# Kernel optimization log

Hardware: AMD Instinct MI355X
Metric: run time of the kernel (lower is better)

## Reference

```python
import jax, jax.numpy as jnp
import numpy as np

DIM = 192
HEADS = 8
TIME = 256
HID = int(DIM * 2.66)  # 510
B, H, W = 4, 128, 128


def conv1x1(x, w, b):
    # w: [O, C], pointwise conv as einsum
    return jnp.einsum('bchw,oc->bohw', x, w) + b[None, :, None, None]


def dwconv3(x, w, b):
    # depthwise 3x3, w: [C, 1, 3, 3]
    y = jax.lax.conv_general_dilated(
        x, w, window_strides=(1, 1), padding='SAME',
        feature_group_count=x.shape[1],
        dimension_numbers=('NCHW', 'OIHW', 'NCHW'))
    return y + b[None, :, None, None]


def layernorm(x, w, b, eps=1e-6):
    # channel-wise LN; torch .std() is unbiased (ddof=1)
    C = x.shape[1]
    mean = x.mean(axis=1, keepdims=True)
    var = ((x - mean) ** 2).sum(axis=1, keepdims=True) / (C - 1)
    std = jnp.sqrt(var)
    return w * (x - mean) / (std + eps) + b


def modulate(x, t_emb, tw, tb):
    # time_mlp = Linear(SiLU(t_emb)); scale/shift conditioning
    t = jax.nn.silu(t_emb) @ tw.T + tb  # [B, 2C]
    scale, shift = jnp.split(t, 2, axis=-1)
    return x * (1.0 + scale[:, :, None, None]) + shift[:, :, None, None]


def l2norm(x, eps=1e-12):
    n = jnp.sqrt((x * x).sum(axis=-1, keepdims=True))
    return x / jnp.maximum(n, eps)


def mdta(x, t_emb, temp, qkv_w, qkv_b, dw_w, dw_b, proj_w, proj_b, tw, tb):
    Bn, C, Hh, Ww = x.shape
    x = modulate(x, t_emb, tw, tb)
    qkv = dwconv3(conv1x1(x, qkv_w, qkv_b), dw_w, dw_b)
    q, k, v = jnp.split(qkv, 3, axis=1)
    rs = lambda a: a.reshape(Bn, HEADS, C // HEADS, Hh * Ww)
    q, k, v = l2norm(rs(q)), l2norm(rs(k)), rs(v)
    attn = jnp.einsum('bhcl,bhdl->bhcd', q, k) * temp[None]  # [B,h,c,c]
    attn = jax.nn.softmax(attn, axis=-1)
    out = jnp.einsum('bhcd,bhdl->bhcl', attn, v).reshape(Bn, C, Hh, Ww)
    return conv1x1(out, proj_w, proj_b)


def gdfn(x, t_emb, c1_w, c1_b, dw_w, dw_b, c2_w, c2_b, tw, tb):
    x = modulate(x, t_emb, tw, tb)
    x = dwconv3(conv1x1(x, c1_w, c1_b), dw_w, dw_b)
    x1, x2 = jnp.split(x, 2, axis=1)
    return conv1x1(x1 * x2, c2_w, c2_b)


def setup_inputs() -> dict:
    key = jax.random.key(0)
    ks = jax.random.split(key, 16)
    s = 0.02
    d = {
        'x': jax.random.normal(ks[0], (B, DIM, H, W), jnp.float32),
        't_emb': jax.random.normal(ks[1], (B, TIME), jnp.float32),
        'n1_w': jnp.ones((1, DIM, 1, 1), jnp.float32),
        'n1_b': jnp.zeros((1, DIM, 1, 1), jnp.float32),
        'temp': jnp.ones((HEADS, 1, 1), jnp.float32),
        'a_qkv_w': jax.random.normal(ks[2], (3 * DIM, DIM), jnp.float32) * s,
        'a_qkv_b': jnp.zeros((3 * DIM,), jnp.float32),
        'a_dw_w': jax.random.normal(ks[3], (3 * DIM, 1, 3, 3), jnp.float32) * s,
        'a_dw_b': jnp.zeros((3 * DIM,), jnp.float32),
        'a_proj_w': jax.random.normal(ks[4], (DIM, DIM), jnp.float32) * s,
        'a_proj_b': jnp.zeros((DIM,), jnp.float32),
        'a_t_w': jax.random.normal(ks[5], (2 * DIM, TIME), jnp.float32) * s,
        'a_t_b': jnp.zeros((2 * DIM,), jnp.float32),
        'n2_w': jnp.ones((1, DIM, 1, 1), jnp.float32),
        'n2_b': jnp.zeros((1, DIM, 1, 1), jnp.float32),
        'f_c1_w': jax.random.normal(ks[6], (2 * HID, DIM), jnp.float32) * s,
        'f_c1_b': jnp.zeros((2 * HID,), jnp.float32),
        'f_dw_w': jax.random.normal(ks[7], (2 * HID, 1, 3, 3), jnp.float32) * s,
        'f_dw_b': jnp.zeros((2 * HID,), jnp.float32),
        'f_c2_w': jax.random.normal(ks[8], (DIM, HID), jnp.float32) * s,
        'f_c2_b': jnp.zeros((DIM,), jnp.float32),
        'f_t_w': jax.random.normal(ks[9], (2 * DIM, TIME), jnp.float32) * s,
        'f_t_b': jnp.zeros((2 * DIM,), jnp.float32),
    }
    return d


def reference(x, t_emb, n1_w, n1_b, temp, a_qkv_w, a_qkv_b, a_dw_w, a_dw_b,
              a_proj_w, a_proj_b, a_t_w, a_t_b, n2_w, n2_b,
              f_c1_w, f_c1_b, f_dw_w, f_dw_b, f_c2_w, f_c2_b, f_t_w, f_t_b):
    x = x + mdta(layernorm(x, n1_w, n1_b), t_emb, temp,
                 a_qkv_w, a_qkv_b, a_dw_w, a_dw_b, a_proj_w, a_proj_b, a_t_w, a_t_b)
    x = x + gdfn(layernorm(x, n2_w, n2_b), t_emb,
                 f_c1_w, f_c1_b, f_dw_w, f_dw_b, f_c2_w, f_c2_b, f_t_w, f_t_b)
    return x
```

## Files before the change

### kernel.cpp

```cpp
#include <hip/hip_runtime.h>
#include <math.h>

#define HW 16384

using short8 = __attribute__((ext_vector_type(8))) short;
using f32x4  = __attribute__((ext_vector_type(4))) float;

__device__ __forceinline__ float bf2f(unsigned short u){
  union { unsigned int i; float f; } x; x.i = ((unsigned int)u) << 16; return x.f;
}
__device__ __forceinline__ unsigned short f2bf(float f){
  union { float f; unsigned int i; } x; x.f = f;
  return (unsigned short)((x.i + 0x7FFFu + ((x.i >> 16) & 1u)) >> 16);
}

__global__ void castw_k(const float* __restrict__ in, unsigned short* __restrict__ out, int n){
  int i = blockIdx.x * 256 + threadIdx.x;
  if (i < n) out[i] = f2bf(in[i]);
}

__global__ void modk(const float* __restrict__ t_emb,
                     const float* __restrict__ aw, const float* __restrict__ ab,
                     const float* __restrict__ fw, const float* __restrict__ fb,
                     float* __restrict__ mod_a, float* __restrict__ mod_f){
  int o = blockIdx.x * 128 + threadIdx.x;
  int b = blockIdx.y;
  const float* w  = blockIdx.z ? fw : aw;
  const float* bi = blockIdx.z ? fb : ab;
  float* outp     = blockIdx.z ? mod_f : mod_a;
  const float* te = t_emb + b * 256;
  float acc = bi[o];
  for (int k = 0; k < 256; ++k){
    float u = te[k];
    float s = u / (1.f + expf(-u));
    acc += s * w[o * 256 + k];
  }
  outp[b * 384 + o] = acc;
}

__global__ __launch_bounds__(256) void lnmod_k(const float* __restrict__ x,
                                               const float* __restrict__ nw, const float* __restrict__ nb,
                                               const float* __restrict__ mod, unsigned short* __restrict__ y){
  int b = blockIdx.y;
  int t = threadIdx.x;
  int pl = t & 63, cg = t >> 6;
  int p = blockIdx.x * 64 + pl;
  const float* xb = x + (size_t)b * 192 * HW + p;
  float s = 0.f, s2 = 0.f;
  #pragma unroll 8
  for (int c = cg * 48; c < cg * 48 + 48; ++c){
    float v = xb[(size_t)c * HW]; s += v; s2 += v * v;
  }
  __shared__ float rs[4][64], rq[4][64];
  rs[cg][pl] = s; rq[cg][pl] = s2;
  __syncthreads();
  float S  = rs[0][pl] + rs[1][pl] + rs[2][pl] + rs[3][pl];
  float S2 = rq[0][pl] + rq[1][pl] + rq[2][pl] + rq[3][pl];
  float mean = S * (1.f / 192.f);
  float var  = (S2 - S * mean) * (1.f / 191.f);
  float rinv = 1.f / (sqrtf(fmaxf(var, 0.f)) + 1e-6f);
  const float* mo = mod + b * 384;
  unsigned short* yb = y + (size_t)b * 192 * HW + p;
  #pragma unroll 8
  for (int c = cg * 48; c < cg * 48 + 48; ++c){
    float v = xb[(size_t)c * HW];
    float ln = nw[c] * ((v - mean) * rinv) + nb[c];
    yb[(size_t)c * HW] = f2bf(ln * (1.f + mo[c]) + mo[192 + c]);
  }
}

#define BM 64
#define BN 128
#define BK 32
__global__ __launch_bounds__(256) void gemm_k(const unsigned short* __restrict__ A,
                                              const unsigned short* __restrict__ Bact,
                                              const float* __restrict__ bias,
                                              const float* resid, void* outp,
                                              int M, int K, int ofp32){
  const int N = HW;
  const unsigned short* Bp = Bact + (size_t)blockIdx.z * K * N;
  int m0 = blockIdx.y * BM, n0 = blockIdx.x * BN;
  __shared__ unsigned short As[BM][40];
  __shared__ unsigned short Bs[BK][136];
  int t = threadIdx.x;
  int wave = t >> 6, lane = t & 63;
  int wr = wave >> 1, wc = wave & 1;
  int l16 = lane & 15, quad = lane >> 4;
  f32x4 z = {0.f, 0.f, 0.f, 0.f};
  f32x4 acc[2][4];
  #pragma unroll
  for (int i = 0; i < 2; ++i)
    #pragma unroll
    for (int j = 0; j < 4; ++j) acc[i][j] = z;

  int kTiles = (K + BK - 1) / BK;
  for (int kt = 0; kt < kTiles; ++kt){
    int k0 = kt * BK;
    {
      int m = t >> 2, kk = (t & 3) * 8;
      int gm = m0 + m;
      #pragma unroll
      for (int j = 0; j < 4; ++j){
        unsigned int v = 0u;
        int gk = k0 + kk + 2 * j;
        if (gm < M && gk < K) v = *(const unsigned int*)(A + (size_t)gm * K + gk);
        *(unsigned int*)&As[m][kk + 2 * j] = v;
      }
    }
    {
      int nn = (t & 15) * 8;
      #pragma unroll
      for (int h2 = 0; h2 < 2; ++h2){
        int r = (t >> 4) + h2 * 16;
        int gk = k0 + r;
        uint4 v; v.x = v.y = v.z = v.w = 0u;
        if (gk < K) v = *(const uint4*)(Bp + (size_t)gk * N + n0 + nn);
        *(uint4*)&Bs[r][nn] = v;
      }
    }
    __syncthreads();
    short8 af[2];
    #pragma unroll
    for (int mt = 0; mt < 2; ++mt)
      af[mt] = *(const short8*)&As[wr * 32 + mt * 16 + l16][quad * 8];
    #pragma unroll
    for (int nt = 0; nt < 4; ++nt){
      int n = wc * 64 + nt * 16 + l16;
      short8 bf;
      #pragma unroll
      for (int j = 0; j < 8; ++j) bf[j] = (short)Bs[quad * 8 + j][n];
      #pragma unroll
      for (int mt = 0; mt < 2; ++mt)
        acc[mt][nt] = __builtin_amdgcn_mfma_f32_16x16x32_bf16(af[mt], bf, acc[mt][nt], 0, 0, 0);
    }
    __syncthreads();
  }
  #pragma unroll
  for (int mt = 0; mt < 2; ++mt)
    #pragma unroll
    for (int nt = 0; nt < 4; ++nt){
      int n = n0 + wc * 64 + nt * 16 + l16;
      #pragma unroll
      for (int r = 0; r < 4; ++r){
        int m = m0 + wr * 32 + mt * 16 + quad * 4 + r;
        if (m < M){
          float v = acc[mt][nt][r] + bias[m];
          size_t idx = (size_t)blockIdx.z * M * N + (size_t)m * N + n;
          if (resid) v += resid[idx];
          if (ofp32) ((float*)outp)[idx] = v;
          else       ((unsigned short*)outp)[idx] = f2bf(v);
        }
      }
    }
}

__global__ __launch_bounds__(256) void dw3_k(const unsigned short* __restrict__ in,
                                             const float* __restrict__ w, const float* __restrict__ bias,
                                             unsigned short* __restrict__ out, int C,
                                             float* __restrict__ qn, float* __restrict__ kn){
  __shared__ unsigned short tile[66 * 128];
  __shared__ float red[4];
  int zc = blockIdx.y;
  int b = zc / C, c = zc - b * C;
  int r0 = blockIdx.x * 64;
  const unsigned short* im = in + ((size_t)(b * C + c)) * HW;
  unsigned short* om = out + ((size_t)(b * C + c)) * HW;
  int t = threadIdx.x;
  #pragma unroll
  for (int i = 0; i < 5; ++i){
    int idx = t + 256 * i;
    if (idx < 1056){
      int lr = idx >> 4, lc = (idx & 15) * 8;
      int gr = r0 - 1 + lr;
      uint4 v = {0u, 0u, 0u, 0u};
      if ((unsigned)gr < 128u) v = *(const uint4*)(im + gr * 128 + lc);
      *(uint4*)&tile[lr * 128 + lc] = v;
    }
  }
  __syncthreads();
  const float* wc = w + c * 9;
  float W[9];
  #pragma unroll
  for (int i = 0; i < 9; ++i) W[i] = wc[i];
  float bs = bias[c];
  float ssq = 0.f;
  #pragma unroll
  for (int i = 0; i < 4; ++i){
    int seg = t + 256 * i;
    int orow = seg >> 4, sc = (seg & 15) * 8;
    float acc[8];
    #pragma unroll
    for (int j = 0; j < 8; ++j) acc[j] = bs;
    #pragma unroll
    for (int rr = 0; rr < 3; ++rr){
      const unsigned short* rp = &tile[(orow + rr) * 128 + sc];
      float v[10];
      v[0] = (sc > 0) ? bf2f(rp[-1]) : 0.f;
      uint4 m = *(const uint4*)rp;
      const unsigned short* mu = (const unsigned short*)&m;
      #pragma unroll
      for (int j = 0; j < 8; ++j) v[j + 1] = bf2f(mu[j]);
      v[9] = (sc < 120) ? bf2f(rp[8]) : 0.f;
      float wa = W[rr * 3], wb = W[rr * 3 + 1], wd = W[rr * 3 + 2];
      #pragma unroll
      for (int j = 0; j < 8; ++j) acc[j] += wa * v[j] + wb * v[j + 1] + wd * v[j + 2];
    }
    unsigned short ob[8];
    #pragma unroll
    for (int j = 0; j < 8; ++j){
      ob[j] = f2bf(acc[j]);
      float q = bf2f(ob[j]);
      ssq += q * q;
    }
    *(uint4*)(om + (r0 + orow) * 128 + sc) = *(uint4*)ob;
  }
  if (c < 384){
    #pragma unroll
    for (int off = 32; off; off >>= 1) ssq += __shfl_down(ssq, off);
    if ((t & 63) == 0) red[t >> 6] = ssq;
    __syncthreads();
    if (t == 0){
      float s = red[0] + red[1] + red[2] + red[3];
      float* dst = (c < 192) ? (qn + b * 192 + c) : (kn + b * 192 + c - 192);
      atomicAdd(dst, s);
    }
  }
}

__global__ __launch_bounds__(256) void dwgate_k(const unsigned short* __restrict__ h,
                                                const float* __restrict__ w, const float* __restrict__ bias,
                                                unsigned short* __restrict__ g){
  __shared__ unsigned short tile[2 * 66 * 128];
  int zc = blockIdx.y;
  int b = zc / 510, j = zc - b * 510;
  int r0 = blockIdx.x * 64;
  const unsigned short* im1 = h + ((size_t)(b * 1020 + j)) * HW;
  const unsigned short* im2 = h + ((size_t)(b * 1020 + 510 + j)) * HW;
  int t = threadIdx.x;
  #pragma unroll
  for (int i = 0; i < 9; ++i){
    int idx = t + 256 * i;
    if (idx < 2112){
      int img = (idx >= 1056) ? 1 : 0;
      int li = idx - img * 1056;
      int lr = li >> 4, lc = (li & 15) * 8;
      int gr = r0 - 1 + lr;
      uint4 v = {0u, 0u, 0u, 0u};
      const unsigned short* im = img ? im2 : im1;
      if ((unsigned)gr < 128u) v = *(const uint4*)(im + gr * 128 + lc);
      *(uint4*)&tile[img * 8448 + lr * 128 + lc] = v;
    }
  }
  __syncthreads();
  float W1[9], W2[9];
  #pragma unroll
  for (int i = 0; i < 9; ++i){ W1[i] = w[j * 9 + i]; W2[i] = w[(510 + j) * 9 + i]; }
  float b1 = bias[j], b2 = bias[510 + j];
  unsigned short* gm = g + ((size_t)(b * 510 + j)) * HW;
  #pragma unroll
  for (int i = 0; i < 4; ++i){
    int seg = t + 256 * i;
    int orow = seg >> 4, sc = (seg & 15) * 8;
    float a1[8], a2[8];
    #pragma unroll
    for (int q = 0; q < 8; ++q){ a1[q] = b1; a2[q] = b2; }
    #pragma unroll
    for (int rr = 0; rr < 3; ++rr){
      #pragma unroll
      for (int img = 0; img < 2; ++img){
        const unsigned short* rp = &tile[img * 8448 + (orow + rr) * 128 + sc];
        float v[10];
        v[0] = (sc > 0) ? bf2f(rp[-1]) : 0.f;
        uint4 m = *(const uint4*)rp;
        const unsigned short* mu = (const unsigned short*)&m;
        #pragma unroll
        for (int q = 0; q < 8; ++q) v[q + 1] = bf2f(mu[q]);
        v[9] = (sc < 120) ? bf2f(rp[8]) : 0.f;
        const float* ww = img ? W2 : W1;
        float* aa = img ? a2 : a1;
        float wa = ww[rr * 3], wb = ww[rr * 3 + 1], wd = ww[rr * 3 + 2];
        #pragma unroll
        for (int q = 0; q < 8; ++q) aa[q] += wa * v[q] + wb * v[q + 1] + wd * v[q + 2];
      }
    }
    unsigned short ob[8];
    #pragma unroll
    for (int q = 0; q < 8; ++q) ob[q] = f2bf(a1[q] * a2[q]);
    *(uint4*)(gm + (r0 + orow) * 128 + sc) = *(uint4*)ob;
  }
}

__global__ __launch_bounds__(64) void qk_k(const unsigned short* __restrict__ qkv_dw, float* __restrict__ part){
  int bh = blockIdx.y; int b = bh >> 3, h = bh & 7;
  int ks = blockIdx.x;
  int lane = threadIdx.x;
  int l16 = lane & 15, quad = lane >> 4;
  const unsigned short* qb = qkv_dw + ((size_t)b * 576 + h * 24) * HW;
  const unsigned short* kb = qkv_dw + ((size_t)b * 576 + 192 + h * 24) * HW;
  f32x4 z = {0.f, 0.f, 0.f, 0.f};
  f32x4 a00 = z, a01 = z, a10 = z, a11 = z;
  for (int st = 0; st < 16; ++st){
    int k0 = ks * 512 + st * 32 + quad * 8;
    short8 qa0 = *(const short8*)(qb + (size_t)l16 * HW + k0);
    short8 qa1 = *(const short8*)(qb + (size_t)(l16 + 16) * HW + k0);
    short8 kb0 = *(const short8*)(kb + (size_t)l16 * HW + k0);
    short8 kb1 = *(const short8*)(kb + (size_t)(l16 + 16) * HW + k0);
    a00 = __builtin_amdgcn_mfma_f32_16x16x32_bf16(qa0, kb0, a00, 0, 0, 0);
    a01 = __builtin_amdgcn_mfma_f32_16x16x32_bf16(qa0, kb1, a01, 0, 0, 0);
    a10 = __builtin_amdgcn_mfma_f32_16x16x32_bf16(qa1, kb0, a10, 0, 0, 0);
    a11 = __builtin_amdgcn_mfma_f32_16x16x32_bf16(qa1, kb1, a11, 0, 0, 0);
  }
  float* pp = part + ((size_t)bh * 32 + ks) * 576;
  #pragma unroll
  for (int r = 0; r < 4; ++r){
    int c0 = quad * 4 + r, c1 = 16 + quad * 4 + r;
    int d0 = l16, d1 = 16 + l16;
    if (c0 < 24 && d0 < 24) pp[c0 * 24 + d0] = a00[r];
    if (c0 < 24 && d1 < 24) pp[c0 * 24 + d1] = a01[r];
    if (c1 < 24 && d0 < 24) pp[c1 * 24 + d0] = a10[r];
    if (c1 < 24 && d1 < 24) pp[c1 * 24 + d1] = a11[r];
  }
}

__global__ void softmax_k(const float* __restrict__ part, const float* __restrict__ qn,
                          const float* __restrict__ kn, const float* __restrict__ temp,
                          float* __restrict__ attn){
  int bh = blockIdx.x; int b = bh >> 3, h = bh & 7;
  int c = threadIdx.x;
  if (c >= 24) return;
  float tmp = temp[h];
  float qv = fmaxf(sqrtf(qn[b * 192 + h * 24 + c]), 1e-12f);
  float row[24];
  #pragma unroll
  for (int d = 0; d < 24; ++d){
    float s = 0.f;
    for (int sp = 0; sp < 32; ++sp) s += part[((size_t)bh * 32 + sp) * 576 + c * 24 + d];
    float kv = fmaxf(sqrtf(kn[b * 192 + h * 24 + d]), 1e-12f);
    row[d] = s * tmp / (qv * kv);
  }
  float mx = row[0];
  #pragma unroll
  for (int d = 1; d < 24; ++d) mx = fmaxf(mx, row[d]);
  float sum = 0.f;
  #pragma unroll
  for (int d = 0; d < 24; ++d){ row[d] = expf(row[d] - mx); sum += row[d]; }
  float inv = 1.f / sum;
  #pragma unroll
  for (int d = 0; d < 24; ++d) attn[(size_t)bh * 576 + c * 24 + d] = row[d] * inv;
}

__global__ __launch_bounds__(256) void av_k(const float* __restrict__ attn,
                                            const unsigned short* __restrict__ qkv_dw,
                                            unsigned short* __restrict__ o){
  int bh = blockIdx.y; int b = bh >> 3, h = bh & 7;
  __shared__ float As[576];
  int t = threadIdx.x;
  for (int i = t; i < 576; i += 256) As[i] = attn[(size_t)bh * 576 + i];
  __syncthreads();
  int p = blockIdx.x * 256 + t;
  const unsigned short* vb = qkv_dw + ((size_t)b * 576 + 384 + h * 24) * HW + p;
  float acc[24];
  #pragma unroll
  for (int c = 0; c < 24; ++c) acc[c] = 0.f;
  #pragma unroll
  for (int d = 0; d < 24; ++d){
    float vv = bf2f(vb[(size_t)d * HW]);
    #pragma unroll
    for (int c = 0; c < 24; ++c) acc[c] += As[c * 24 + d] * vv;
  }
  unsigned short* ob = o + ((size_t)b * 192 + h * 24) * HW + p;
  #pragma unroll
  for (int c = 0; c < 24; ++c) ob[(size_t)c * HW] = f2bf(acc[c]);
}

extern "C" void kernel_launch(void* const* d_in, const int* in_sizes, int n_in,
                              void* d_out, int out_size, void* d_ws, size_t ws_size,
                              hipStream_t stream){
  (void)in_sizes; (void)n_in; (void)out_size; (void)ws_size;
  const float* x        = (const float*)d_in[0];
  const float* t_emb    = (const float*)d_in[1];
  const float* n1_w     = (const float*)d_in[2];
  const float* n1_b     = (const float*)d_in[3];
  const float* temp     = (const float*)d_in[4];
  const float* a_qkv_w  = (const float*)d_in[5];
  const float* a_qkv_b  = (const float*)d_in[6];
  const float* a_dw_w   = (const float*)d_in[7];
  const float* a_dw_b   = (const float*)d_in[8];
  const float* a_proj_w = (const float*)d_in[9];
  const float* a_proj_b = (const float*)d_in[10];
  const float* a_t_w    = (const float*)d_in[11];
  const float* a_t_b    = (const float*)d_in[12];
  const float* n2_w     = (const float*)d_in[13];
  const float* n2_b     = (const float*)d_in[14];
  const float* f_c1_w   = (const float*)d_in[15];
  const float* f_c1_b   = (const float*)d_in[16];
  const float* f_dw_w   = (const float*)d_in[17];
  const float* f_dw_b   = (const float*)d_in[18];
  const float* f_c2_w   = (const float*)d_in[19];
  const float* f_c2_b   = (const float*)d_in[20];
  const float* f_t_w    = (const float*)d_in[21];
  const float* f_t_b    = (const float*)d_in[22];
  float* out = (float*)d_out;
  char* ws = (char*)d_ws;

  unsigned short* y_buf = (unsigned short*)(ws + 0);
  unsigned short* qkv   = (unsigned short*)(ws + 25165824);
  unsigned short* hbuf  = (unsigned short*)(ws + 25165824);
  unsigned short* qkvd  = (unsigned short*)(ws + 100663296);
  unsigned short* obuf  = (unsigned short*)(ws + 176160768);
  unsigned short* gbuf  = (unsigned short*)(ws + 158859264);
  const size_t S = 225705984;
  float* mod_a = (float*)(ws + S);
  float* mod_f = (float*)(ws + S + 8192);
  float* qn    = (float*)(ws + S + 16384);
  float* kn    = (float*)(ws + S + 20480);
  float* part  = (float*)(ws + S + 24576);
  float* attn  = (float*)(ws + S + 2383872);
  unsigned short* Wq = (unsigned short*)(ws + S + 2457600);
  unsigned short* Wp = (unsigned short*)(ws + S + 2678784);
  unsigned short* W1 = (unsigned short*)(ws + S + 2752512);
  unsigned short* W2 = (unsigned short*)(ws + S + 3144192);

  castw_k<<<dim3((110592 + 255) / 256), 256, 0, stream>>>(a_qkv_w, Wq, 110592);
  castw_k<<<dim3((36864 + 255) / 256), 256, 0, stream>>>(a_proj_w, Wp, 36864);
  castw_k<<<dim3((195840 + 255) / 256), 256, 0, stream>>>(f_c1_w, W1, 195840);
  castw_k<<<dim3((97920 + 255) / 256), 256, 0, stream>>>(f_c2_w, W2, 97920);
  modk<<<dim3(3, 4, 2), 128, 0, stream>>>(t_emb, a_t_w, a_t_b, f_t_w, f_t_b, mod_a, mod_f);
  hipMemsetAsync(qn, 0, 2 * 768 * sizeof(float), stream);

  lnmod_k<<<dim3(256, 4), 256, 0, stream>>>(x, n1_w, n1_b, mod_a, y_buf);
  gemm_k<<<dim3(128, 9, 4), 256, 0, stream>>>(Wq, y_buf, a_qkv_b, nullptr, qkv, 576, 192, 0);
  dw3_k<<<dim3(2, 2304), 256, 0, stream>>>(qkv, a_dw_w, a_dw_b, qkvd, 576, qn, kn);
  qk_k<<<dim3(32, 32), 64, 0, stream>>>(qkvd, part);
  softmax_k<<<32, 64, 0, stream>>>(part, qn, kn, temp, attn);
  av_k<<<dim3(64, 32), 256, 0, stream>>>(attn, qkvd, obuf);
  gemm_k<<<dim3(128, 3, 4), 256, 0, stream>>>(Wp, obuf, a_proj_b, x, out, 192, 192, 1);

  lnmod_k<<<dim3(256, 4), 256, 0, stream>>>(out, n2_w, n2_b, mod_f, y_buf);
  gemm_k<<<dim3(128, 16, 4), 256, 0, stream>>>(W1, y_buf, f_c1_b, nullptr, hbuf, 1020, 192, 0);
  dwgate_k<<<dim3(2, 2040), 256, 0, stream>>>(hbuf, f_dw_w, f_dw_b, gbuf);
  gemm_k<<<dim3(128, 3, 4), 256, 0, stream>>>(W2, gbuf, f_c2_b, out, out, 192, 510, 1);
}
```

Measured before the change: 821.1 us.

## Switch GEMM activations to pixel-major layout with K-contiguous TN GEMM

```diff
diff --git a/kernel.cpp b/kernel.cpp
--- a/kernel.cpp
+++ b/kernel.cpp
@@ -17,6 +17,14 @@
 __global__ void castw_k(const float* __restrict__ in, unsigned short* __restrict__ out, int n){
   int i = blockIdx.x * 256 + threadIdx.x;
   if (i < n) out[i] = f2bf(in[i]);
+}
+__global__ void castw_pad_k(const float* __restrict__ in, unsigned short* __restrict__ out,
+                            int M, int Kin, int Kout){
+  int i = blockIdx.x * 256 + threadIdx.x;
+  if (i < M * Kout){
+    int m = i / Kout, k = i - m * Kout;
+    out[i] = (k < Kin) ? f2bf(in[m * Kin + k]) : (unsigned short)0;
+  }
 }
 
 __global__ void modk(const float* __restrict__ t_emb,
@@ -60,89 +68,76 @@
   float var  = (S2 - S * mean) * (1.f / 191.f);
   float rinv = 1.f / (sqrtf(fmaxf(var, 0.f)) + 1e-6f);
   const float* mo = mod + b * 384;
-  unsigned short* yb = y + (size_t)b * 192 * HW + p;
+  unsigned short buf[48];
   #pragma unroll 8
-  for (int c = cg * 48; c < cg * 48 + 48; ++c){
+  for (int i = 0; i < 48; ++i){
+    int c = cg * 48 + i;
     float v = xb[(size_t)c * HW];
     float ln = nw[c] * ((v - mean) * rinv) + nb[c];
-    yb[(size_t)c * HW] = f2bf(ln * (1.f + mo[c]) + mo[192 + c]);
-  }
-}
-
-#define BM 64
-#define BN 128
-#define BK 32
-__global__ __launch_bounds__(256) void gemm_k(const unsigned short* __restrict__ A,
-                                              const unsigned short* __restrict__ Bact,
-                                              const float* __restrict__ bias,
-                                              const float* resid, void* outp,
-                                              int M, int K, int ofp32){
+    buf[i] = f2bf(ln * (1.f + mo[c]) + mo[192 + c]);
+  }
+  unsigned short* yb = y + ((size_t)b * HW + p) * 192 + cg * 48;
+  #pragma unroll
+  for (int i = 0; i < 6; ++i) *(uint4*)(yb + i * 8) = *(const uint4*)(buf + i * 8);
+}
+
+__global__ __launch_bounds__(256) void gemm_tn(const unsigned short* __restrict__ A,
+                                               const unsigned short* __restrict__ Bact,
+                                               const float* __restrict__ bias,
+                                               const float* resid, void* outp,
+                                               int M, int K, int ofp32){
   const int N = HW;
-  const unsigned short* Bp = Bact + (size_t)blockIdx.z * K * N;
-  int m0 = blockIdx.y * BM, n0 = blockIdx.x * BN;
-  __shared__ unsigned short As[BM][40];
-  __shared__ unsigned short Bs[BK][136];
-  int t = threadIdx.x;
-  int wave = t >> 6, lane = t & 63;
-  int wr = wave >> 1, wc = wave & 1;
+  const unsigned short* Bp = Bact + (size_t)blockIdx.z * N * K;
+  int m0 = blockIdx.x * 64, n0 = blockIdx.y * 256;
+  __shared__ unsigned short As[64 * 32];
+  __shared__ unsigned short Bs[256 * 32];
+  int t = threadIdx.x;
+  int w = t >> 6, lane = t & 63;
   int l16 = lane & 15, quad = lane >> 4;
   f32x4 z = {0.f, 0.f, 0.f, 0.f};
-  f32x4 acc[2][4];
-  #pragma unroll
-  for (int i = 0; i < 2; ++i)
+  f32x4 acc[4][4];
+  #pragma unroll
+  for (int i = 0; i < 4; ++i)
     #pragma unroll
     for (int j = 0; j < 4; ++j) acc[i][j] = z;
 
-  int kTiles = (K + BK - 1) / BK;
+  int kTiles = K >> 5;
   for (int kt = 0; kt < kTiles; ++kt){
-    int k0 = kt * BK;
+    int k0 = kt * 32;
     {
-      int m = t >> 2, kk = (t & 3) * 8;
-      int gm = m0 + m;
+      int row = t >> 2, kc = t & 3;
+      int gm = m0 + row; if (gm > M - 1) gm = M - 1;
+      *(uint4*)&As[row * 32 + kc * 8] = *(const uint4*)(A + (size_t)gm * K + k0 + kc * 8);
+    }
+    #pragma unroll
+    for (int i = 0; i < 4; ++i){
+      int id = t + 256 * i;
+      int row = id >> 2, kc = id & 3;
+      *(uint4*)&Bs[row * 32 + kc * 8] = *(const uint4*)(Bp + (size_t)(n0 + row) * K + k0 + kc * 8);
+    }
+    __syncthreads();
+    short8 af[4], bfr[4];
+    #pragma unroll
+    for (int mt = 0; mt < 4; ++mt)
+      af[mt] = *(const short8*)&As[(mt * 16 + l16) * 32 + quad * 8];
+    #pragma unroll
+    for (int nt = 0; nt < 4; ++nt)
+      bfr[nt] = *(const short8*)&Bs[(w * 64 + nt * 16 + l16) * 32 + quad * 8];
+    #pragma unroll
+    for (int nt = 0; nt < 4; ++nt)
       #pragma unroll
-      for (int j = 0; j < 4; ++j){
-        unsigned int v = 0u;
-        int gk = k0 + kk + 2 * j;
-        if (gm < M && gk < K) v = *(const unsigned int*)(A + (size_t)gm * K + gk);
-        *(unsigned int*)&As[m][kk + 2 * j] = v;
-      }
-    }
-    {
-      int nn = (t & 15) * 8;
-      #pragma unroll
-      for (int h2 = 0; h2 < 2; ++h2){
-        int r = (t >> 4) + h2 * 16;
-        int gk = k0 + r;
-        uint4 v; v.x = v.y = v.z = v.w = 0u;
-        if (gk < K) v = *(const uint4*)(Bp + (size_t)gk * N + n0 + nn);
-        *(uint4*)&Bs[r][nn] = v;
-      }
-    }
+      for (int mt = 0; mt < 4; ++mt)
+        acc[mt][nt] = __builtin_amdgcn_mfma_f32_16x16x32_bf16(af[mt], bfr[nt], acc[mt][nt], 0, 0, 0);
     __syncthreads();
-    short8 af[2];
-    #pragma unroll
-    for (int mt = 0; mt < 2; ++mt)
-      af[mt] = *(const short8*)&As[wr * 32 + mt * 16 + l16][quad * 8];
+  }
+  #pragma unroll
+  for (int mt = 0; mt < 4; ++mt)
     #pragma unroll
     for (int nt = 0; nt < 4; ++nt){
-      int n = wc * 64 + nt * 16 + l16;
-      short8 bf;
-      #pragma unroll
-      for (int j = 0; j < 8; ++j) bf[j] = (short)Bs[quad * 8 + j][n];
-      #pragma unroll
-      for (int mt = 0; mt < 2; ++mt)
-        acc[mt][nt] = __builtin_amdgcn_mfma_f32_16x16x32_bf16(af[mt], bf, acc[mt][nt], 0, 0, 0);
-    }
-    __syncthreads();
-  }
-  #pragma unroll
-  for (int mt = 0; mt < 2; ++mt)
-    #pragma unroll
-    for (int nt = 0; nt < 4; ++nt){
-      int n = n0 + wc * 64 + nt * 16 + l16;
+      int n = n0 + w * 64 + nt * 16 + l16;
       #pragma unroll
       for (int r = 0; r < 4; ++r){
-        int m = m0 + wr * 32 + mt * 16 + quad * 4 + r;
+        int m = m0 + mt * 16 + quad * 4 + r;
         if (m < M){
           float v = acc[mt][nt][r] + bias[m];
           size_t idx = (size_t)blockIdx.z * M * N + (size_t)m * N + n;
@@ -287,6 +282,31 @@
     #pragma unroll
     for (int q = 0; q < 8; ++q) ob[q] = f2bf(a1[q] * a2[q]);
     *(uint4*)(gm + (r0 + orow) * 128 + sc) = *(uint4*)ob;
+  }
+}
+
+__global__ __launch_bounds__(256) void tr_k(const unsigned short* __restrict__ in,
+                                            unsigned short* __restrict__ out, int C, int Kout){
+  __shared__ unsigned short tile[64 * 72];
+  int b = blockIdx.z;
+  int p0 = blockIdx.x * 64, c0 = blockIdx.y * 64;
+  int t = threadIdx.x;
+  #pragma unroll
+  for (int i = 0; i < 2; ++i){
+    int id = t + 256 * i;
+    int ch = id >> 3, pc = (id & 7) * 8;
+    uint4 v = {0u, 0u, 0u, 0u};
+    if (c0 + ch < C) v = *(const uint4*)(in + ((size_t)(b * C + c0 + ch)) * HW + p0 + pc);
+    const unsigned short* u = (const unsigned short*)&v;
+    #pragma unroll
+    for (int j = 0; j < 8; ++j) tile[(pc + j) * 72 + ch] = u[j];
+  }
+  __syncthreads();
+  #pragma unroll
+  for (int i = 0; i < 2; ++i){
+    int id = t + 256 * i;
+    int px = id >> 3, cc = (id & 7) * 8;
+    *(uint4*)(out + ((size_t)b * HW + p0 + px) * Kout + c0 + cc) = *(const uint4*)&tile[px * 72 + cc];
   }
 }
 
@@ -368,9 +388,12 @@
     #pragma unroll
     for (int c = 0; c < 24; ++c) acc[c] += As[c * 24 + d] * vv;
   }
-  unsigned short* ob = o + ((size_t)b * 192 + h * 24) * HW + p;
-  #pragma unroll
-  for (int c = 0; c < 24; ++c) ob[(size_t)c * HW] = f2bf(acc[c]);
+  unsigned short ob[24];
+  #pragma unroll
+  for (int c = 0; c < 24; ++c) ob[c] = f2bf(acc[c]);
+  unsigned short* op = o + ((size_t)b * HW + p) * 192 + h * 24;
+  #pragma unroll
+  for (int i = 0; i < 3; ++i) *(uint4*)(op + i * 8) = *(const uint4*)(ob + i * 8);
 }
 
 extern "C" void kernel_launch(void* const* d_in, const int* in_sizes, int n_in,
@@ -406,6 +429,7 @@
   unsigned short* y_buf = (unsigned short*)(ws + 0);
   unsigned short* qkv   = (unsigned short*)(ws + 25165824);
   unsigned short* hbuf  = (unsigned short*)(ws + 25165824);
+  unsigned short* gbufT = (unsigned short*)(ws + 25165824);
   unsigned short* qkvd  = (unsigned short*)(ws + 100663296);
   unsigned short* obuf  = (unsigned short*)(ws + 176160768);
   unsigned short* gbuf  = (unsigned short*)(ws + 158859264);
@@ -416,28 +440,29 @@
   float* kn    = (float*)(ws + S + 20480);
   float* part  = (float*)(ws + S + 24576);
   float* attn  = (float*)(ws + S + 2383872);
-  unsigned short* Wq = (unsigned short*)(ws + S + 2457600);
-  unsigned short* Wp = (unsigned short*)(ws + S + 2678784);
-  unsigned short* W1 = (unsigned short*)(ws + S + 2752512);
-  unsigned short* W2 = (unsigned short*)(ws + S + 3144192);
+  unsigned short* Wq  = (unsigned short*)(ws + S + 2457600);
+  unsigned short* Wp  = (unsigned short*)(ws + S + 2678784);
+  unsigned short* W1  = (unsigned short*)(ws + S + 2752512);
+  unsigned short* W2p = (unsigned short*)(ws + S + 3144192);
 
   castw_k<<<dim3((110592 + 255) / 256), 256, 0, stream>>>(a_qkv_w, Wq, 110592);
   castw_k<<<dim3((36864 + 255) / 256), 256, 0, stream>>>(a_proj_w, Wp, 36864);
   castw_k<<<dim3((195840 + 255) / 256), 256, 0, stream>>>(f_c1_w, W1, 195840);
-  castw_k<<<dim3((97920 + 255) / 256), 256, 0, stream>>>(f_c2_w, W2, 97920);
+  castw_pad_k<<<dim3((98304 + 255) / 256), 256, 0, stream>>>(f_c2_w, W2p, 192, 510, 512);
   modk<<<dim3(3, 4, 2), 128, 0, stream>>>(t_emb, a_t_w, a_t_b, f_t_w, f_t_b, mod_a, mod_f);
   hipMemsetAsync(qn, 0, 2 * 768 * sizeof(float), stream);
 
   lnmod_k<<<dim3(256, 4), 256, 0, stream>>>(x, n1_w, n1_b, mod_a, y_buf);
-  gemm_k<<<dim3(128, 9, 4), 256, 0, stream>>>(Wq, y_buf, a_qkv_b, nullptr, qkv, 576, 192, 0);
+  gemm_tn<<<dim3(9, 64, 4), 256, 0, stream>>>(Wq, y_buf, a_qkv_b, nullptr, qkv, 576, 192, 0);
   dw3_k<<<dim3(2, 2304), 256, 0, stream>>>(qkv, a_dw_w, a_dw_b, qkvd, 576, qn, kn);
   qk_k<<<dim3(32, 32), 64, 0, stream>>>(qkvd, part);
   softmax_k<<<32, 64, 0, stream>>>(part, qn, kn, temp, attn);
   av_k<<<dim3(64, 32), 256, 0, stream>>>(attn, qkvd, obuf);
-  gemm_k<<<dim3(128, 3, 4), 256, 0, stream>>>(Wp, obuf, a_proj_b, x, out, 192, 192, 1);
+  gemm_tn<<<dim3(3, 64, 4), 256, 0, stream>>>(Wp, obuf, a_proj_b, x, out, 192, 192, 1);
 
   lnmod_k<<<dim3(256, 4), 256, 0, stream>>>(out, n2_w, n2_b, mod_f, y_buf);
-  gemm_k<<<dim3(128, 16, 4), 256, 0, stream>>>(W1, y_buf, f_c1_b, nullptr, hbuf, 1020, 192, 0);
+  gemm_tn<<<dim3(16, 64, 4), 256, 0, stream>>>(W1, y_buf, f_c1_b, nullptr, hbuf, 1020, 192, 0);
   dwgate_k<<<dim3(2, 2040), 256, 0, stream>>>(hbuf, f_dw_w, f_dw_b, gbuf);
-  gemm_k<<<dim3(128, 3, 4), 256, 0, stream>>>(W2, gbuf, f_c2_b, out, out, 192, 510, 1);
-}
+  tr_k<<<dim3(256, 8, 4), 256, 0, stream>>>(gbuf, gbufT, 510, 512);
+  gemm_tn<<<dim3(3, 64, 4), 256, 0, stream>>>(W2p, gbufT, f_c2_b, out, out, 192, 512, 1);
+}
```

Measured after the change: 796.8 us. 1.03x faster.
